# Optimization experiments

Measured on AMD Instinct MI355X. Metric: run time of the kernel, lower is better.

## Reference

```python
import jax, jax.numpy as jnp
import numpy as np

CHUNK_SIZE = 256


def setup_inputs() -> dict:
    key = jax.random.key(0)
    kq, kk, kv = jax.random.split(key, 3)
    b, h, L, d, dv = 2, 16, 4096, 16, 64
    return {
        "q": jax.random.normal(kq, (b, h, L, d), dtype=jnp.float32),
        "k": jax.random.normal(kk, (b, h, L, d), dtype=jnp.float32),
        "v": jax.random.normal(kv, (b, h, L, dv), dtype=jnp.float32),
    }


def reference(q, k, v):
    b, h, L, d = q.shape
    dv = v.shape[-1]
    cs = CHUNK_SIZE
    n = L // cs

    q = q * d ** (-0.5)

    # ---- normalizer z over full sequence ----
    k_cumsum = jnp.cumsum(k, axis=-2)                               # [b,h,L,d]
    kk_cumsum = jnp.cumsum(k[..., :, None] * k[..., None, :], axis=-3)  # [b,h,L,d,d]
    z = (q * k_cumsum).sum(-1)
    z = z + 0.5 * jnp.einsum('bhld,bhle,bhlde->bhl', q, q, kk_cumsum)
    z = z + (jnp.arange(L, dtype=z.dtype) + 1.0)[None, None, :]

    # ---- zeroth-order term ----
    o_const = jnp.cumsum(v, axis=-2)                                # [b,h,L,dv]

    # ---- chunked view ----
    qc = q.reshape(b, h, n, cs, d)
    kc = k.reshape(b, h, n, cs, d)
    vc = v.reshape(b, h, n, cs, dv)

    # intra-chunk quadratic attention: S + 0.5*S^2, causal-masked
    s = jnp.einsum('bhnqd,bhnkd->bhnqk', qc, kc)                    # [b,h,n,cs,cs]
    s = s + 0.5 * s ** 2
    causal_mask = jnp.tril(jnp.ones((cs, cs), dtype=bool))
    s = jnp.where(causal_mask, s, jnp.zeros((), dtype=s.dtype))
    o = jnp.einsum('bhnqk,bhnkf->bhnqf', s, vc)                     # [b,h,n,cs,dv]

    # inter-chunk quadratic state: cumulative K x K x V from previous chunks
    kv_quad = jnp.einsum('bhncd,bhnce,bhncf->bhndef', kc, kc, vc)   # [b,h,n,d,d,dv]
    kv_quad = jnp.cumsum(kv_quad, axis=2)
    kv_quad = jnp.concatenate(
        [jnp.zeros_like(kv_quad[:, :, :1]), kv_quad[:, :, :-1]], axis=2)
    o = o + 0.5 * jnp.einsum('bhndef,bhncd,bhnce->bhncf', kv_quad, qc, qc)

    # inter-chunk linear state: cumulative K x V from previous chunks
    kv_lin = jnp.einsum('bhncd,bhnce->bhnde', kc, vc)               # [b,h,n,d,dv]
    kv_lin = jnp.cumsum(kv_lin, axis=2)
    kv_lin = jnp.concatenate(
        [jnp.zeros_like(kv_lin[:, :, :1]), kv_lin[:, :, :-1]], axis=2)
    o = o + jnp.einsum('bhnde,bhncd->bhnce', kv_lin, qc)

    o = o.reshape(b, h, L, dv) + o_const
    return o / (z[..., None] + 1e-6)
```

## Files before the change

### kernel.cpp

```cpp
#include <hip/hip_runtime.h>
#include <hip/hip_cooperative_groups.h>
#include <cstddef>

#define BH    32
#define LSEQ  4096
#define D     16
#define DV    64
#define CS    256
#define NC    16
#define NF    160
#define NZ    65
#define KSTEPS 5
#define PER   (NZ * NF)

typedef short short8 __attribute__((ext_vector_type(8)));
typedef float f32x4 __attribute__((ext_vector_type(4)));
typedef float f4 __attribute__((ext_vector_type(4)));
typedef unsigned uint4v __attribute__((ext_vector_type(4)));

#define OFF_KBF 0u
#define OFF_VT  (4u*1024u*1024u)
#define OFF_ST  (OFF_VT + (unsigned)(BH*NZ*LSEQ*2))

__device__ __forceinline__ unsigned f2bf(float x) {
  unsigned u = __float_as_uint(x);
  return (u + 0x7FFFu + ((u >> 16) & 1u)) >> 16;
}
__device__ __forceinline__ float bf2f(unsigned short u) {
  return __uint_as_float(((unsigned)u) << 16);
}
__device__ __forceinline__ short8 zero8() {
  short8 z = {0,0,0,0,0,0,0,0};
  return z;
}
__device__ __forceinline__ unsigned cvtpk(float lo, float hi) {
  unsigned r;
  asm("v_cvt_pk_bf16_f32 %0, %1, %2" : "=v"(r) : "v"(lo), "v"(hi));
  return r;
}
__device__ __forceinline__ short8 pk4(unsigned a, unsigned b, unsigned c, unsigned d) {
  uint4v u = {a, b, c, d};
  return __builtin_bit_cast(short8, u);
}

__device__ __forceinline__ unsigned feat_tbl(int f) {
  if (f == 0)  return 16u | (16u << 8);
  if (f <= 16) return (unsigned)(f - 1) | (16u << 8);
  if (f < 137) {
    int p = f - 17, off = 0;
    for (int d = 0; d < 15; ++d) {
      int cnt = 15 - d;
      if (p < off + cnt) return (unsigned)d | ((unsigned)(d + 1 + p - off) << 8);
      off += cnt;
    }
  }
  if (f < 153) {
    int d = f - 137;
    return (unsigned)d | ((unsigned)d << 8) | (1u << 16);
  }
  return 17u | (17u << 8);
}

struct Smem {
  float kxqx[CS][18];
  __align__(16) unsigned short vt[NZ][264];
  union {
    __align__(16) unsigned short stt[NZ][168];
    struct {
      __align__(16) unsigned short ptile[8][640];
      float zline[CS];
    } u;
  } b;
  unsigned tbl[NF];
};

__global__ __launch_bounds__(512, 4) void unified(const float* __restrict__ q,
                                                  const float* __restrict__ k,
                                                  const float* __restrict__ v,
                                                  unsigned* __restrict__ kbf_u32,
                                                  unsigned short* __restrict__ st,
                                                  float* __restrict__ out) {
  __shared__ Smem sm;
  int blk = blockIdx.x, bh = blk >> 4, c = blk & 15;
  int t = threadIdx.x, w = t >> 6, lane = t & 63, quad = lane >> 4, n16 = lane & 15;
  const size_t base = (size_t)bh * LSEQ + (size_t)c * CS;

  {
    const f4* K4 = (const f4*)(k + base * D);
    uint2* kbd2 = (uint2*)(kbf_u32 + base * D / 2);
    for (int idx = t; idx < 1024; idx += 512) {
      f4 kv = K4[idx];
      kbd2[idx] = make_uint2(cvtpk(kv[0], kv[1]), cvtpk(kv[2], kv[3]));
      float* dst = &sm.kxqx[idx >> 2][(idx & 3) * 4];
      *(float2*)dst = make_float2(kv[0], kv[1]);
      *(float2*)(dst + 2) = make_float2(kv[2], kv[3]);
    }
    for (int i = t; i < CS; i += 512)
      *(float2*)&sm.kxqx[i][16] = make_float2(1.f, 0.f);
    const f4* V4 = (const f4*)(v + base * DV);
    for (int idx = t; idx < 2048; idx += 512) {
      int m16 = idx & 15, j0 = (idx >> 4) * 2;
      f4 a  = V4[j0 * 16 + m16];
      f4 bq = V4[j0 * 16 + 16 + m16];
#pragma unroll
      for (int r = 0; r < 4; ++r)
        *(unsigned*)&sm.vt[m16 * 4 + r][j0] = cvtpk(a[r], bq[r]);
    }
    if (t < 128) ((unsigned*)&sm.vt[64][0])[t] = 0x3F803F80u;
    if (t < NF) sm.tbl[t] = feat_tbl(t);
  }
  __syncthreads();

  if (c < 15 && w < 5) {
    unsigned tv0 = sm.tbl[(w * 2 + 0) * 16 + n16];
    unsigned tv1 = sm.tbl[(w * 2 + 1) * 16 + n16];
    int d0 = tv0 & 255, e0 = (tv0 >> 8) & 255;
    int d1 = tv1 & 255, e1 = (tv1 >> 8) & 255;
    f32x4 acc[2][5];
#pragma unroll
    for (int mm = 0; mm < 2; ++mm)
#pragma unroll
      for (int nt = 0; nt < 5; ++nt) acc[mm][nt] = (f32x4){0.f, 0.f, 0.f, 0.f};
    for (int jt = 0; jt < 8; ++jt) {
      float x0[8], x1[8];
#pragma unroll
      for (int i = 0; i < 8; ++i) {
        const float* kr = &sm.kxqx[jt * 32 + quad * 8 + i][0];
        x0[i] = kr[d0] * kr[e0];
        x1[i] = kr[d1] * kr[e1];
      }
      short8 afr0 = pk4(cvtpk(x0[0], x0[1]), cvtpk(x0[2], x0[3]),
                        cvtpk(x0[4], x0[5]), cvtpk(x0[6], x0[7]));
      short8 afr1 = pk4(cvtpk(x1[0], x1[1]), cvtpk(x1[2], x1[3]),
                        cvtpk(x1[4], x1[5]), cvtpk(x1[6], x1[7]));
#pragma unroll
      for (int nt = 0; nt < 5; ++nt) {
        int ncol = nt * 16 + n16;
        short8 b = zero8();
        if (ncol < NZ) b = *(const short8*)(&sm.vt[ncol][jt * 32 + quad * 8]);
        acc[0][nt] = __builtin_amdgcn_mfma_f32_16x16x32_bf16(afr0, b, acc[0][nt], 0, 0, 0);
        acc[1][nt] = __builtin_amdgcn_mfma_f32_16x16x32_bf16(afr1, b, acc[1][nt], 0, 0, 0);
      }
    }
    unsigned short* stc = st + (size_t)(bh * NC + c) * PER;
#pragma unroll
    for (int mm = 0; mm < 2; ++mm) {
      int feat0 = (w * 2 + mm) * 16 + quad * 4;
      float sc[4];
#pragma unroll
      for (int r = 0; r < 4; ++r)
        sc[r] = (feat0 + r >= 137 && feat0 + r < 153) ? 0.5f : 1.0f;
#pragma unroll
      for (int nt = 0; nt < 5; ++nt) {
        int col = nt * 16 + n16;
        if (col < NZ) {
          unsigned lo = cvtpk(acc[mm][nt][0] * sc[0], acc[mm][nt][1] * sc[1]);
          unsigned hi = cvtpk(acc[mm][nt][2] * sc[2], acc[mm][nt][3] * sc[3]);
          *(uint2*)(stc + (size_t)col * NF + feat0) = make_uint2(lo, hi);
        }
      }
    }
  }
  __syncthreads();

  {
    const f4* Q4 = (const f4*)(q + base * D);
    for (int idx = t; idx < 1024; idx += 512) {
      f4 qv = Q4[idx] * 0.25f;
      float* dst = &sm.kxqx[idx >> 2][(idx & 3) * 4];
      *(float2*)dst = make_float2(qv[0], qv[1]);
      *(float2*)(dst + 2) = make_float2(qv[2], qv[3]);
    }
  }

  cooperative_groups::this_grid().sync();

  if (c > 0) {
    const unsigned short* stg = st + (size_t)bh * NC * PER;
    float s0[8], s1[8], s2[8];
#pragma unroll
    for (int e = 0; e < 8; ++e) { s0[e] = 0.f; s1[e] = 0.f; s2[e] = 0.f; }
    const int i0 = t * 8, i1 = i0 + 4096, i2 = i0 + 8192;
    const bool h2 = (i2 < PER);
    for (int cc = 0; cc < c; ++cc) {
      const unsigned short* pcc = stg + (size_t)cc * PER;
      short8 a0 = *(const short8*)(pcc + i0);
      short8 a1 = *(const short8*)(pcc + i1);
      short8 a2 = h2 ? *(const short8*)(pcc + i2) : zero8();
#pragma unroll
      for (int e = 0; e < 8; ++e) {
        s0[e] += bf2f((unsigned short)a0[e]);
        s1[e] += bf2f((unsigned short)a1[e]);
        s2[e] += bf2f((unsigned short)a2[e]);
      }
    }
    {
      int col = i0 / NF, ft = i0 - col * NF;
      *(short8*)(&sm.b.stt[col][ft]) =
          pk4(cvtpk(s0[0], s0[1]), cvtpk(s0[2], s0[3]),
              cvtpk(s0[4], s0[5]), cvtpk(s0[6], s0[7]));
      col = i1 / NF; ft = i1 - col * NF;
      *(short8*)(&sm.b.stt[col][ft]) =
          pk4(cvtpk(s1[0], s1[1]), cvtpk(s1[2], s1[3]),
              cvtpk(s1[4], s1[5]), cvtpk(s1[6], s1[7]));
      if (h2) {
        col = i2 / NF; ft = i2 - col * NF;
        *(short8*)(&sm.b.stt[col][ft]) =
            pk4(cvtpk(s2[0], s2[1]), cvtpk(s2[2], s2[3]),
                cvtpk(s2[4], s2[5]), cvtpk(s2[6], s2[7]));
      }
    }
  }
  __syncthreads();

  f32x4 acc[2][5];
#pragma unroll
  for (int mm = 0; mm < 2; ++mm)
#pragma unroll
    for (int nt = 0; nt < 5; ++nt) acc[mm][nt] = (f32x4){0.f, 0.f, 0.f, 0.f};

  if (c > 0) {
    const float* qrow0 = &sm.kxqx[w * 16 + n16][0];
    const float* qrow1 = &sm.kxqx[(15 - w) * 16 + n16][0];
    for (int ks = 0; ks < KSTEPS; ++ks) {
      unsigned tvv[8];
#pragma unroll
      for (int i = 0; i < 8; ++i) tvv[i] = sm.tbl[ks * 32 + quad * 8 + i];
      float x0[8], x1[8];
#pragma unroll
      for (int i = 0; i < 8; ++i) {
        int d = tvv[i] & 255, e = (tvv[i] >> 8) & 255;
        x0[i] = qrow0[d] * qrow0[e];
        x1[i] = qrow1[d] * qrow1[e];
      }
      short8 afr0 = pk4(cvtpk(x0[0], x0[1]), cvtpk(x0[2], x0[3]),
                        cvtpk(x0[4], x0[5]), cvtpk(x0[6], x0[7]));
      short8 afr1 = pk4(cvtpk(x1[0], x1[1]), cvtpk(x1[2], x1[3]),
                        cvtpk(x1[4], x1[5]), cvtpk(x1[6], x1[7]));
#pragma unroll
      for (int nt = 0; nt < 5; ++nt) {
        int ncol = nt * 16 + n16;
        short8 b = zero8();
        if (ncol < NZ) b = *(const short8*)(&sm.b.stt[ncol][ks * 32 + quad * 8]);
        acc[0][nt] = __builtin_amdgcn_mfma_f32_16x16x32_bf16(afr0, b, acc[0][nt], 0, 0, 0);
        acc[1][nt] = __builtin_amdgcn_mfma_f32_16x16x32_bf16(afr1, b, acc[1][nt], 0, 0, 0);
      }
    }
  }
  __syncthreads();

  const unsigned short* kbc = (const unsigned short*)kbf_u32 + base * D;
  unsigned short* pw = &sm.b.u.ptile[w][0];
  short8 ones;
#pragma unroll
  for (int i = 0; i < 8; ++i) ones[i] = (short)0x3F80;

#pragma unroll
  for (int mm = 0; mm < 2; ++mm) {
    const int s = mm ? (15 - w) : w;
    short8 qf = zero8();
    if (quad < 2) {
      const float2* qr = (const float2*)&sm.kxqx[s * 16 + n16][quad * 8];
      float2 q0 = qr[0], q1 = qr[1], q2 = qr[2], q3 = qr[3];
      qf = pk4(cvtpk(q0.x, q0.y), cvtpk(q1.x, q1.y),
               cvtpk(q2.x, q2.y), cvtpk(q3.x, q3.y));
    }
    const int ntiles = (s >> 1) + 1;
    for (int jt = 0; jt < ntiles; ++jt) {
      short8 kb[2];
#pragma unroll
      for (int ntk = 0; ntk < 2; ++ntk) {
        short8 b = zero8();
        if (quad < 2)
          b = *(const short8*)(kbc + (size_t)(jt * 32 + ntk * 16 + n16) * D + quad * 8);
        kb[ntk] = b;
      }
      f32x4 zf = (f32x4){0.f, 0.f, 0.f, 0.f};
      f32x4 sres[2];
      sres[0] = __builtin_amdgcn_mfma_f32_16x16x32_bf16(qf, kb[0], zf, 0, 0, 0);
      sres[1] = __builtin_amdgcn_mfma_f32_16x16x32_bf16(qf, kb[1], zf, 0, 0, 0);
      const bool last = (jt == ntiles - 1);
#pragma unroll
      for (int ntk = 0; ntk < 2; ++ntk) {
        float ph[4];
#pragma unroll
        for (int r = 0; r < 4; ++r) {
          float sv = sres[ntk][r];
          float phi = fmaf(sv, fmaf(0.5f, sv, 1.0f), 1.0f);
          if (last) {
            int qrow_g = s * 16 + quad * 4 + r;
            int kcol_g = jt * 32 + ntk * 16 + n16;
            if (kcol_g > qrow_g) phi = 0.f;
          }
          ph[r] = phi;
        }
        unsigned u01 = cvtpk(ph[0], ph[1]);
        unsigned u23 = cvtpk(ph[2], ph[3]);
        int rb = (quad * 4) * 40 + ntk * 16 + n16;
        pw[rb      ] = (unsigned short)u01;
        pw[rb +  40] = (unsigned short)(u01 >> 16);
        pw[rb +  80] = (unsigned short)u23;
        pw[rb + 120] = (unsigned short)(u23 >> 16);
      }
      short8 pa = *(const short8*)(pw + n16 * 40 + quad * 8);
#pragma unroll
      for (int nt = 0; nt < 5; ++nt) {
        int ncol = nt * 16 + n16;
        short8 b;
        if (ncol < 64)       b = *(const short8*)(&sm.vt[ncol][jt * 32 + quad * 8]);
        else if (ncol == 64) b = ones;
        else                 b = zero8();
        acc[mm][nt] = __builtin_amdgcn_mfma_f32_16x16x32_bf16(pa, b, acc[mm][nt], 0, 0, 0);
      }
    }
  }

  if (n16 == 0) {
#pragma unroll
    for (int mm = 0; mm < 2; ++mm) {
      int s = mm ? (15 - w) : w;
#pragma unroll
      for (int r = 0; r < 4; ++r)
        sm.b.u.zline[s * 16 + quad * 4 + r] = acc[mm][4][r];
    }
  }
  float* oc = out + base * DV;
#pragma unroll
  for (int mm = 0; mm < 2; ++mm) {
    int s = mm ? (15 - w) : w;
#pragma unroll
    for (int r = 0; r < 4; ++r) {
      int qrow = s * 16 + quad * 4 + r;
      float inv = __builtin_amdgcn_rcpf(sm.b.u.zline[qrow] + 1e-6f);
#pragma unroll
      for (int nt = 0; nt < 4; ++nt)
        oc[(size_t)qrow * DV + nt * 16 + n16] = acc[mm][nt][r] * inv;
    }
  }
}

__global__ __launch_bounds__(320) void pass_a(const float* __restrict__ k,
                                              const float* __restrict__ v,
                                              unsigned* __restrict__ kbf_u32,
                                              unsigned* __restrict__ vt_u32,
                                              unsigned short* __restrict__ st) {
  __shared__ float kx[CS][18];
  __shared__ __align__(16) unsigned short vt_lds[NZ][264];
  __shared__ unsigned tbl[NF];
  int blk = blockIdx.x, bh = blk >> 4, c = blk & 15;
  int t = threadIdx.x, w = t >> 6, lane = t & 63, quad = lane >> 4, n16 = lane & 15;
  {
    const float2* kc2 = (const float2*)(k + ((size_t)bh * LSEQ + c * CS) * D);
    unsigned* kbd = kbf_u32 + ((size_t)bh * LSEQ + c * CS) * D / 2;
    for (int i = t; i < 2048; i += 320) {
      float2 v2 = kc2[i];
      kbd[i] = f2bf(v2.x) | (f2bf(v2.y) << 16);
      int j = i >> 3, dd = (i & 7) * 2;
      kx[j][dd] = v2.x; kx[j][dd + 1] = v2.y;
    }
    for (int i = t; i < CS; i += 320) { kx[i][16] = 1.f; kx[i][17] = 0.f; }
  }
  {
    const float* vb = v + ((size_t)bh * LSEQ + c * CS) * DV;
    for (int i = t; i < CS * DV; i += 320) {
      int j = i >> 6, f = i & 63;
      vt_lds[f][j] = (unsigned short)f2bf(vb[i]);
    }
    for (int i = t; i < CS; i += 320) vt_lds[64][i] = (unsigned short)0x3F80;
  }
  if (t < NF) tbl[t] = feat_tbl(t);
  __syncthreads();
  {
    unsigned* vtg = vt_u32 + (size_t)bh * NZ * (LSEQ / 2) + c * (CS / 2);
    for (int i = t; i < NZ * (CS / 2); i += 320) {
      int f = i >> 7, jp = (i & 127) * 2;
      vtg[(size_t)f * (LSEQ / 2) + (i & 127)] =
          (unsigned)vt_lds[f][jp] | ((unsigned)vt_lds[f][jp + 1] << 16);
    }
  }
  f32x4 acc[2][5];
#pragma unroll
  for (int mm = 0; mm < 2; ++mm)
#pragma unroll
    for (int nt = 0; nt < 5; ++nt) acc[mm][nt] = (f32x4){0.f, 0.f, 0.f, 0.f};
  for (int jt = 0; jt < 8; ++jt) {
    short8 afr[2];
#pragma unroll
    for (int mm = 0; mm < 2; ++mm) {
      int feat = (w * 2 + mm) * 16 + n16;
      unsigned tv = tbl[feat];
      int d = tv & 255, e = (tv >> 8) & 255;
      short8 a;
#pragma unroll
      for (int i = 0; i < 8; ++i) {
        int jj = jt * 32 + quad * 8 + i;
        a[i] = (short)f2bf(kx[jj][d] * kx[jj][e]);
      }
      afr[mm] = a;
    }
#pragma unroll
    for (int nt = 0; nt < 5; ++nt) {
      int ncol = nt * 16 + n16;
      short8 b = zero8();
      if (ncol < NZ) b = *(const short8*)(&vt_lds[ncol][jt * 32 + quad * 8]);
      acc[0][nt] = __builtin_amdgcn_mfma_f32_16x16x32_bf16(afr[0], b, acc[0][nt], 0, 0, 0);
      acc[1][nt] = __builtin_amdgcn_mfma_f32_16x16x32_bf16(afr[1], b, acc[1][nt], 0, 0, 0);
    }
  }
  unsigned short* stc = st + (size_t)(bh * NC + c) * PER;
#pragma unroll
  for (int mm = 0; mm < 2; ++mm)
#pragma unroll
    for (int nt = 0; nt < 5; ++nt) {
      int col = nt * 16 + n16;
      if (col < NZ) {
        unsigned lo = f2bf(acc[mm][nt][0]) | (f2bf(acc[mm][nt][1]) << 16);
        unsigned hi = f2bf(acc[mm][nt][2]) | (f2bf(acc[mm][nt][3]) << 16);
        int feat0 = (w * 2 + mm) * 16 + quad * 4;
        *(uint2*)(stc + (size_t)col * NF + feat0) = make_uint2(lo, hi);
      }
    }
}

__global__ __launch_bounds__(256) void pass_b(unsigned short* __restrict__ st) {
  const int TOT = BH * PER;
  int idx = blockIdx.x * 256 + threadIdx.x;
  if (idx >= TOT) return;
  int bh = idx / PER, r = idx - bh * PER;
  unsigned short* p = st + (size_t)bh * NC * PER + r;
  float run = 0.f;
#pragma unroll
  for (int c = 0; c < NC; ++c) {
    unsigned short uv = p[(size_t)c * PER];
    float val = bf2f(uv);
    p[(size_t)c * PER] = (unsigned short)f2bf(run);
    run += val;
  }
}

__global__ __launch_bounds__(512) void pass_c(const float* __restrict__ q,
                                              const unsigned short* __restrict__ kbf,
                                              const unsigned short* __restrict__ vt,
                                              const unsigned short* __restrict__ st,
                                              float* __restrict__ out) {
  __shared__ float qx[CS][18];
  __shared__ unsigned tbl[NF];
  __shared__ __align__(16) unsigned short ptile[8][32 * 40];
  __shared__ float zline[CS];
  int blk = blockIdx.x, bh = blk >> 4, c = blk & 15;
  const size_t base = (size_t)bh * LSEQ + (size_t)c * CS;
  const float* qc = q + base * D;
  int t = threadIdx.x, w = t >> 6, lane = t & 63, quad = lane >> 4, n16 = lane & 15;
  for (int i = t; i < CS * D; i += 512) {
    int row = i >> 4, dd = i & 15;
    qx[row][dd] = qc[i] * 0.25f;
  }
  for (int i = t; i < CS; i += 512) { qx[i][16] = 1.f; qx[i][17] = 0.f; }
  if (t < NF) tbl[t] = feat_tbl(t);
  __syncthreads();
  f32x4 acc[2][5];
#pragma unroll
  for (int mm = 0; mm < 2; ++mm)
#pragma unroll
    for (int nt = 0; nt < 5; ++nt) acc[mm][nt] = (f32x4){0.f, 0.f, 0.f, 0.f};
  if (c > 0) {
    const unsigned short* stc = st + (size_t)(bh * NC + c) * PER;
    for (int ks = 0; ks < KSTEPS; ++ks) {
      short8 afr[2];
#pragma unroll
      for (int mm = 0; mm < 2; ++mm) {
        const float* qrow = qx[(w * 2 + mm) * 16 + n16];
        short8 a;
#pragma unroll
        for (int i = 0; i < 8; ++i) {
          int f = ks * 32 + quad * 8 + i;
          unsigned tv = tbl[f];
          float val = qrow[tv & 255] * qrow[(tv >> 8) & 255];
          if (tv & 0x10000u) val *= 0.5f;
          a[i] = (short)f2bf(val);
        }
        afr[mm] = a;
      }
#pragma unroll
      for (int nt = 0; nt < 5; ++nt) {
        int ncol = nt * 16 + n16;
        short8 b = zero8();
        if (ncol < NZ) b = *(const short8*)(stc + (size_t)ncol * NF + ks * 32 + quad * 8);
        acc[0][nt] = __builtin_amdgcn_mfma_f32_16x16x32_bf16(afr[0], b, acc[0][nt], 0, 0, 0);
        acc[1][nt] = __builtin_amdgcn_mfma_f32_16x16x32_bf16(afr[1], b, acc[1][nt], 0, 0, 0);
      }
    }
  }
  short8 qfr[2];
#pragma unroll
  for (int mm = 0; mm < 2; ++mm) {
    int m = (w * 2 + mm) * 16 + n16;
    short8 a = zero8();
    if (quad < 2) {
#pragma unroll
      for (int i = 0; i < 8; ++i) a[i] = (short)f2bf(qx[m][quad * 8 + i]);
    }
    qfr[mm] = a;
  }
  const unsigned short* kbc = kbf + base * D;
  const unsigned short* vtb = vt + (size_t)bh * NZ * LSEQ + (size_t)c * CS;
  unsigned short* pw = &ptile[w][0];
  short8 ones;
#pragma unroll
  for (int i = 0; i < 8; ++i) ones[i] = (short)0x3F80;
  for (int jt = 0; jt <= w; ++jt) {
    short8 kb[2];
#pragma unroll
    for (int ntk = 0; ntk < 2; ++ntk) {
      short8 b = zero8();
      if (quad < 2)
        b = *(const short8*)(kbc + (size_t)(jt * 32 + ntk * 16 + n16) * D + quad * 8);
      kb[ntk] = b;
    }
    f32x4 zf = (f32x4){0.f, 0.f, 0.f, 0.f};
    f32x4 s[2][2];
#pragma unroll
    for (int mm = 0; mm < 2; ++mm)
#pragma unroll
      for (int ntk = 0; ntk < 2; ++ntk)
        s[mm][ntk] = __builtin_amdgcn_mfma_f32_16x16x32_bf16(qfr[mm], kb[ntk], zf, 0, 0, 0);
    bool diag = (jt == w);
#pragma unroll
    for (int mm = 0; mm < 2; ++mm)
#pragma unroll
      for (int ntk = 0; ntk < 2; ++ntk)
#pragma unroll
        for (int r = 0; r < 4; ++r) {
          float sv = s[mm][ntk][r];
          float phi = fmaf(0.5f * sv, sv, sv) + 1.0f;
          if (diag) {
            int qrow = mm * 16 + quad * 4 + r;
            int kcol = ntk * 16 + n16;
            if (kcol > qrow) phi = 0.f;
          }
          pw[(mm * 16 + quad * 4 + r) * 40 + ntk * 16 + n16] = (unsigned short)f2bf(phi);
        }
    short8 pa[2];
#pragma unroll
    for (int mm = 0; mm < 2; ++mm)
      pa[mm] = *(const short8*)(pw + (mm * 16 + n16) * 40 + quad * 8);
#pragma unroll
    for (int nt = 0; nt < 5; ++nt) {
      int ncol = nt * 16 + n16;
      short8 b;
      if (ncol < 64)       b = *(const short8*)(vtb + (size_t)ncol * LSEQ + jt * 32 + quad * 8);
      else if (ncol == 64) b = ones;
      else                 b = zero8();
      acc[0][nt] = __builtin_amdgcn_mfma_f32_16x16x32_bf16(pa[0], b, acc[0][nt], 0, 0, 0);
      acc[1][nt] = __builtin_amdgcn_mfma_f32_16x16x32_bf16(pa[1], b, acc[1][nt], 0, 0, 0);
    }
  }
  if (n16 == 0) {
#pragma unroll
    for (int mm = 0; mm < 2; ++mm)
#pragma unroll
      for (int r = 0; r < 4; ++r)
        zline[(w * 2 + mm) * 16 + quad * 4 + r] = acc[mm][4][r];
  }
  float* oc = out + base * DV;
#pragma unroll
  for (int mm = 0; mm < 2; ++mm)
#pragma unroll
    for (int r = 0; r < 4; ++r) {
      int qrow = (w * 2 + mm) * 16 + quad * 4 + r;
      float inv = 1.0f / (zline[qrow] + 1e-6f);
#pragma unroll
      for (int nt = 0; nt < 4; ++nt)
        oc[(size_t)qrow * DV + nt * 16 + n16] = acc[mm][nt][r] * inv;
    }
}

extern "C" void kernel_launch(void* const* d_in, const int* in_sizes, int n_in,
                              void* d_out, int out_size, void* d_ws, size_t ws_size,
                              hipStream_t stream) {
  (void)in_sizes; (void)n_in; (void)out_size; (void)ws_size;
  const float* q = (const float*)d_in[0];
  const float* k = (const float*)d_in[1];
  const float* v = (const float*)d_in[2];
  float* out = (float*)d_out;
  char* wsb = (char*)d_ws;
  unsigned*       kbf32 = (unsigned*)(wsb + OFF_KBF);
  unsigned short* kbf   = (unsigned short*)(wsb + OFF_KBF);
  unsigned*       vt32  = (unsigned*)(wsb + OFF_VT);
  unsigned short* vtp   = (unsigned short*)(wsb + OFF_VT);
  unsigned short* stp   = (unsigned short*)(wsb + OFF_ST);

  int nb = 0;
  hipError_t oe = hipOccupancyMaxActiveBlocksPerMultiprocessor(
      &nb, reinterpret_cast<const void*>(unified), 512, 0);
  if (oe == hipSuccess && nb >= 2) {
    void* args[] = {(void*)&q, (void*)&k, (void*)&v,
                    (void*)&kbf32, (void*)&stp, (void*)&out};
    hipLaunchCooperativeKernel(reinterpret_cast<const void*>(unified),
                               dim3(BH * NC), dim3(512), args, 0, stream);
  } else {
    pass_a<<<BH * NC, 320, 0, stream>>>(k, v, kbf32, vt32, stp);
    pass_b<<<1300, 256, 0, stream>>>(stp);
    pass_c<<<BH * NC, 512, 0, stream>>>(q, kbf, vtp, stp, out);
  }
}
```

Before: 135.2 us.

## Move intra-chunk attention before grid sync and rebalance state work across waves

The intra-chunk causal attention now runs before the cooperative grid barrier, computed from K held in LDS instead of a bf16 K copy in global memory, so the global K write is dropped. Q fragments are loaded straight from global into registers at kernel start. Chunk-state feature tiles are spread over all 8 waves (waves 0-1 take two tiles), and query-row slices are reassigned so causal work is balanced per wave. The prefix-sum loop over earlier chunk states is software-pipelined with one-ahead loads. The accumulators now stay live across the grid sync, which raises register pressure.

```diff
diff --git a/kernel.cpp b/kernel.cpp
--- a/kernel.cpp
+++ b/kernel.cpp
@@ -84,13 +84,28 @@
   int blk = blockIdx.x, bh = blk >> 4, c = blk & 15;
   int t = threadIdx.x, w = t >> 6, lane = t & 63, quad = lane >> 4, n16 = lane & 15;
   const size_t base = (size_t)bh * LSEQ + (size_t)c * CS;
+  (void)kbf_u32;
+
+  const int s0 = (w < 2) ? 2 * w : (w + 2);
+  const int s1 = (w < 2) ? 2 * w + 1 : (17 - w);
+
+  short8 qf[2] = {zero8(), zero8()};
+  if (quad < 2) {
+#pragma unroll
+    for (int mm = 0; mm < 2; ++mm) {
+      int s = mm ? s1 : s0;
+      const f4* qp = (const f4*)(q + (base + (size_t)(s * 16 + n16)) * D + quad * 8);
+      f4 qa = qp[0] * 0.25f;
+      f4 qb = qp[1] * 0.25f;
+      qf[mm] = pk4(cvtpk(qa[0], qa[1]), cvtpk(qa[2], qa[3]),
+                   cvtpk(qb[0], qb[1]), cvtpk(qb[2], qb[3]));
+    }
+  }
 
   {
     const f4* K4 = (const f4*)(k + base * D);
-    uint2* kbd2 = (uint2*)(kbf_u32 + base * D / 2);
     for (int idx = t; idx < 1024; idx += 512) {
       f4 kv = K4[idx];
-      kbd2[idx] = make_uint2(cvtpk(kv[0], kv[1]), cvtpk(kv[2], kv[3]));
       float* dst = &sm.kxqx[idx >> 2][(idx & 3) * 4];
       *(float2*)dst = make_float2(kv[0], kv[1]);
       *(float2*)(dst + 2) = make_float2(kv[2], kv[3]);
@@ -111,41 +126,34 @@
   }
   __syncthreads();
 
-  if (c < 15 && w < 5) {
-    unsigned tv0 = sm.tbl[(w * 2 + 0) * 16 + n16];
-    unsigned tv1 = sm.tbl[(w * 2 + 1) * 16 + n16];
-    int d0 = tv0 & 255, e0 = (tv0 >> 8) & 255;
-    int d1 = tv1 & 255, e1 = (tv1 >> 8) & 255;
-    f32x4 acc[2][5];
-#pragma unroll
-    for (int mm = 0; mm < 2; ++mm)
-#pragma unroll
-      for (int nt = 0; nt < 5; ++nt) acc[mm][nt] = (f32x4){0.f, 0.f, 0.f, 0.f};
-    for (int jt = 0; jt < 8; ++jt) {
-      float x0[8], x1[8];
-#pragma unroll
-      for (int i = 0; i < 8; ++i) {
-        const float* kr = &sm.kxqx[jt * 32 + quad * 8 + i][0];
-        x0[i] = kr[d0] * kr[e0];
-        x1[i] = kr[d1] * kr[e1];
-      }
-      short8 afr0 = pk4(cvtpk(x0[0], x0[1]), cvtpk(x0[2], x0[3]),
-                        cvtpk(x0[4], x0[5]), cvtpk(x0[6], x0[7]));
-      short8 afr1 = pk4(cvtpk(x1[0], x1[1]), cvtpk(x1[2], x1[3]),
-                        cvtpk(x1[4], x1[5]), cvtpk(x1[6], x1[7]));
-#pragma unroll
-      for (int nt = 0; nt < 5; ++nt) {
-        int ncol = nt * 16 + n16;
-        short8 b = zero8();
-        if (ncol < NZ) b = *(const short8*)(&sm.vt[ncol][jt * 32 + quad * 8]);
-        acc[0][nt] = __builtin_amdgcn_mfma_f32_16x16x32_bf16(afr0, b, acc[0][nt], 0, 0, 0);
-        acc[1][nt] = __builtin_amdgcn_mfma_f32_16x16x32_bf16(afr1, b, acc[1][nt], 0, 0, 0);
-      }
-    }
+  if (c < 15) {
+    const int ntt = (w < 2) ? 2 : 1;
     unsigned short* stc = st + (size_t)(bh * NC + c) * PER;
-#pragma unroll
-    for (int mm = 0; mm < 2; ++mm) {
-      int feat0 = (w * 2 + mm) * 16 + quad * 4;
+    for (int tt = 0; tt < ntt; ++tt) {
+      const int T = tt ? (w + 8) : w;
+      unsigned tv = sm.tbl[T * 16 + n16];
+      int d0 = tv & 255, e0 = (tv >> 8) & 255;
+      f32x4 acc5[5];
+#pragma unroll
+      for (int nt = 0; nt < 5; ++nt) acc5[nt] = (f32x4){0.f, 0.f, 0.f, 0.f};
+      for (int jt = 0; jt < 8; ++jt) {
+        float x[8];
+#pragma unroll
+        for (int i = 0; i < 8; ++i) {
+          const float* kr = &sm.kxqx[jt * 32 + quad * 8 + i][0];
+          x[i] = kr[d0] * kr[e0];
+        }
+        short8 afr = pk4(cvtpk(x[0], x[1]), cvtpk(x[2], x[3]),
+                         cvtpk(x[4], x[5]), cvtpk(x[6], x[7]));
+#pragma unroll
+        for (int nt = 0; nt < 5; ++nt) {
+          int ncol = nt * 16 + n16;
+          short8 b = zero8();
+          if (ncol < NZ) b = *(const short8*)(&sm.vt[ncol][jt * 32 + quad * 8]);
+          acc5[nt] = __builtin_amdgcn_mfma_f32_16x16x32_bf16(afr, b, acc5[nt], 0, 0, 0);
+        }
+      }
+      const int feat0 = T * 16 + quad * 4;
       float sc[4];
 #pragma unroll
       for (int r = 0; r < 4; ++r)
@@ -154,9 +162,80 @@
       for (int nt = 0; nt < 5; ++nt) {
         int col = nt * 16 + n16;
         if (col < NZ) {
-          unsigned lo = cvtpk(acc[mm][nt][0] * sc[0], acc[mm][nt][1] * sc[1]);
-          unsigned hi = cvtpk(acc[mm][nt][2] * sc[2], acc[mm][nt][3] * sc[3]);
+          unsigned lo = cvtpk(acc5[nt][0] * sc[0], acc5[nt][1] * sc[1]);
+          unsigned hi = cvtpk(acc5[nt][2] * sc[2], acc5[nt][3] * sc[3]);
           *(uint2*)(stc + (size_t)col * NF + feat0) = make_uint2(lo, hi);
+        }
+      }
+    }
+  }
+
+  f32x4 accC[2][5];
+#pragma unroll
+  for (int mm = 0; mm < 2; ++mm)
+#pragma unroll
+    for (int nt = 0; nt < 5; ++nt) accC[mm][nt] = (f32x4){0.f, 0.f, 0.f, 0.f};
+
+  {
+    unsigned short* pw = &sm.b.u.ptile[w][0];
+    short8 ones;
+#pragma unroll
+    for (int i = 0; i < 8; ++i) ones[i] = (short)0x3F80;
+
+#pragma unroll
+    for (int mm = 0; mm < 2; ++mm) {
+      const int s = mm ? s1 : s0;
+      const int ntiles = (s >> 1) + 1;
+      for (int jt = 0; jt < ntiles; ++jt) {
+        short8 kb[2];
+#pragma unroll
+        for (int ntk = 0; ntk < 2; ++ntk) {
+          short8 b = zero8();
+          if (quad < 2) {
+            const float2* kr =
+                (const float2*)&sm.kxqx[jt * 32 + ntk * 16 + n16][quad * 8];
+            float2 k0 = kr[0], k1 = kr[1], k2 = kr[2], k3 = kr[3];
+            b = pk4(cvtpk(k0.x, k0.y), cvtpk(k1.x, k1.y),
+                    cvtpk(k2.x, k2.y), cvtpk(k3.x, k3.y));
+          }
+          kb[ntk] = b;
+        }
+        f32x4 zf = (f32x4){0.f, 0.f, 0.f, 0.f};
+        f32x4 sres[2];
+        sres[0] = __builtin_amdgcn_mfma_f32_16x16x32_bf16(qf[mm], kb[0], zf, 0, 0, 0);
+        sres[1] = __builtin_amdgcn_mfma_f32_16x16x32_bf16(qf[mm], kb[1], zf, 0, 0, 0);
+        const bool last = (jt == ntiles - 1);
+#pragma unroll
+        for (int ntk = 0; ntk < 2; ++ntk) {
+          float ph[4];
+#pragma unroll
+          for (int r = 0; r < 4; ++r) {
+            float sv = sres[ntk][r];
+            float phi = fmaf(sv, fmaf(0.5f, sv, 1.0f), 1.0f);
+            if (last) {
+              int qrow_g = s * 16 + quad * 4 + r;
+              int kcol_g = jt * 32 + ntk * 16 + n16;
+              if (kcol_g > qrow_g) phi = 0.f;
+            }
+            ph[r] = phi;
+          }
+          unsigned u01 = cvtpk(ph[0], ph[1]);
+          unsigned u23 = cvtpk(ph[2], ph[3]);
+          int rb = (quad * 4) * 40 + ntk * 16 + n16;
+          pw[rb      ] = (unsigned short)u01;
+          pw[rb +  40] = (unsigned short)(u01 >> 16);
+          pw[rb +  80] = (unsigned short)u23;
+          pw[rb + 120] = (unsigned short)(u23 >> 16);
+        }
+        short8 pa = *(const short8*)(pw + n16 * 40 + quad * 8);
+#pragma unroll
+        for (int nt = 0; nt < 5; ++nt) {
+          int ncol = nt * 16 + n16;
+          short8 b;
+          if (ncol < 64)       b = *(const short8*)(&sm.vt[ncol][jt * 32 + quad * 8]);
+          else if (ncol == 64) b = ones;
+          else                 b = zero8();
+          accC[mm][nt] = __builtin_amdgcn_mfma_f32_16x16x32_bf16(pa, b, accC[mm][nt], 0, 0, 0);
         }
       }
     }
@@ -177,51 +256,55 @@
 
   if (c > 0) {
     const unsigned short* stg = st + (size_t)bh * NC * PER;
-    float s0[8], s1[8], s2[8];
-#pragma unroll
-    for (int e = 0; e < 8; ++e) { s0[e] = 0.f; s1[e] = 0.f; s2[e] = 0.f; }
+    float sa0[8], sa1[8], sa2[8];
+#pragma unroll
+    for (int e = 0; e < 8; ++e) { sa0[e] = 0.f; sa1[e] = 0.f; sa2[e] = 0.f; }
     const int i0 = t * 8, i1 = i0 + 4096, i2 = i0 + 8192;
     const bool h2 = (i2 < PER);
-    for (int cc = 0; cc < c; ++cc) {
-      const unsigned short* pcc = stg + (size_t)cc * PER;
-      short8 a0 = *(const short8*)(pcc + i0);
-      short8 a1 = *(const short8*)(pcc + i1);
-      short8 a2 = h2 ? *(const short8*)(pcc + i2) : zero8();
+    short8 a0 = *(const short8*)(stg + i0);
+    short8 a1 = *(const short8*)(stg + i1);
+    short8 a2 = h2 ? *(const short8*)(stg + i2) : zero8();
+    for (int cc = 1; cc < c; ++cc) {
+      const unsigned short* pn = stg + (size_t)cc * PER;
+      short8 b0 = *(const short8*)(pn + i0);
+      short8 b1 = *(const short8*)(pn + i1);
+      short8 b2 = h2 ? *(const short8*)(pn + i2) : zero8();
 #pragma unroll
       for (int e = 0; e < 8; ++e) {
-        s0[e] += bf2f((unsigned short)a0[e]);
-        s1[e] += bf2f((unsigned short)a1[e]);
-        s2[e] += bf2f((unsigned short)a2[e]);
-      }
+        sa0[e] += bf2f((unsigned short)a0[e]);
+        sa1[e] += bf2f((unsigned short)a1[e]);
+        sa2[e] += bf2f((unsigned short)a2[e]);
+      }
+      a0 = b0; a1 = b1; a2 = b2;
+    }
+#pragma unroll
+    for (int e = 0; e < 8; ++e) {
+      sa0[e] += bf2f((unsigned short)a0[e]);
+      sa1[e] += bf2f((unsigned short)a1[e]);
+      sa2[e] += bf2f((unsigned short)a2[e]);
     }
     {
       int col = i0 / NF, ft = i0 - col * NF;
       *(short8*)(&sm.b.stt[col][ft]) =
-          pk4(cvtpk(s0[0], s0[1]), cvtpk(s0[2], s0[3]),
-              cvtpk(s0[4], s0[5]), cvtpk(s0[6], s0[7]));
+          pk4(cvtpk(sa0[0], sa0[1]), cvtpk(sa0[2], sa0[3]),
+              cvtpk(sa0[4], sa0[5]), cvtpk(sa0[6], sa0[7]));
       col = i1 / NF; ft = i1 - col * NF;
       *(short8*)(&sm.b.stt[col][ft]) =
-          pk4(cvtpk(s1[0], s1[1]), cvtpk(s1[2], s1[3]),
-              cvtpk(s1[4], s1[5]), cvtpk(s1[6], s1[7]));
+          pk4(cvtpk(sa1[0], sa1[1]), cvtpk(sa1[2], sa1[3]),
+              cvtpk(sa1[4], sa1[5]), cvtpk(sa1[6], sa1[7]));
       if (h2) {
         col = i2 / NF; ft = i2 - col * NF;
         *(short8*)(&sm.b.stt[col][ft]) =
-            pk4(cvtpk(s2[0], s2[1]), cvtpk(s2[2], s2[3]),
-                cvtpk(s2[4], s2[5]), cvtpk(s2[6], s2[7]));
+            pk4(cvtpk(sa2[0], sa2[1]), cvtpk(sa2[2], sa2[3]),
+                cvtpk(sa2[4], sa2[5]), cvtpk(sa2[6], sa2[7]));
       }
     }
   }
   __syncthreads();
 
-  f32x4 acc[2][5];
-#pragma unroll
-  for (int mm = 0; mm < 2; ++mm)
-#pragma unroll
-    for (int nt = 0; nt < 5; ++nt) acc[mm][nt] = (f32x4){0.f, 0.f, 0.f, 0.f};
-
   if (c > 0) {
-    const float* qrow0 = &sm.kxqx[w * 16 + n16][0];
-    const float* qrow1 = &sm.kxqx[(15 - w) * 16 + n16][0];
+    const float* qrow0 = &sm.kxqx[s0 * 16 + n16][0];
+    const float* qrow1 = &sm.kxqx[s1 * 16 + n16][0];
     for (int ks = 0; ks < KSTEPS; ++ks) {
       unsigned tvv[8];
 #pragma unroll
@@ -242,99 +325,33 @@
         int ncol = nt * 16 + n16;
         short8 b = zero8();
         if (ncol < NZ) b = *(const short8*)(&sm.b.stt[ncol][ks * 32 + quad * 8]);
-        acc[0][nt] = __builtin_amdgcn_mfma_f32_16x16x32_bf16(afr0, b, acc[0][nt], 0, 0, 0);
-        acc[1][nt] = __builtin_amdgcn_mfma_f32_16x16x32_bf16(afr1, b, acc[1][nt], 0, 0, 0);
+        accC[0][nt] = __builtin_amdgcn_mfma_f32_16x16x32_bf16(afr0, b, accC[0][nt], 0, 0, 0);
+        accC[1][nt] = __builtin_amdgcn_mfma_f32_16x16x32_bf16(afr1, b, accC[1][nt], 0, 0, 0);
       }
     }
   }
   __syncthreads();
 
-  const unsigned short* kbc = (const unsigned short*)kbf_u32 + base * D;
-  unsigned short* pw = &sm.b.u.ptile[w][0];
-  short8 ones;
-#pragma unroll
-  for (int i = 0; i < 8; ++i) ones[i] = (short)0x3F80;
-
+  if (n16 == 0) {
+#pragma unroll
+    for (int mm = 0; mm < 2; ++mm) {
+      int s = mm ? s1 : s0;
+#pragma unroll
+      for (int r = 0; r < 4; ++r)
+        sm.b.u.zline[s * 16 + quad * 4 + r] = accC[mm][4][r];
+    }
+  }
+  float* oc = out + base * DV;
 #pragma unroll
   for (int mm = 0; mm < 2; ++mm) {
-    const int s = mm ? (15 - w) : w;
-    short8 qf = zero8();
-    if (quad < 2) {
-      const float2* qr = (const float2*)&sm.kxqx[s * 16 + n16][quad * 8];
-      float2 q0 = qr[0], q1 = qr[1], q2 = qr[2], q3 = qr[3];
-      qf = pk4(cvtpk(q0.x, q0.y), cvtpk(q1.x, q1.y),
-               cvtpk(q2.x, q2.y), cvtpk(q3.x, q3.y));
-    }
-    const int ntiles = (s >> 1) + 1;
-    for (int jt = 0; jt < ntiles; ++jt) {
-      short8 kb[2];
-#pragma unroll
-      for (int ntk = 0; ntk < 2; ++ntk) {
-        short8 b = zero8();
-        if (quad < 2)
-          b = *(const short8*)(kbc + (size_t)(jt * 32 + ntk * 16 + n16) * D + quad * 8);
-        kb[ntk] = b;
-      }
-      f32x4 zf = (f32x4){0.f, 0.f, 0.f, 0.f};
-      f32x4 sres[2];
-      sres[0] = __builtin_amdgcn_mfma_f32_16x16x32_bf16(qf, kb[0], zf, 0, 0, 0);
-      sres[1] = __builtin_amdgcn_mfma_f32_16x16x32_bf16(qf, kb[1], zf, 0, 0, 0);
-      const bool last = (jt == ntiles - 1);
-#pragma unroll
-      for (int ntk = 0; ntk < 2; ++ntk) {
-        float ph[4];
-#pragma unroll
-        for (int r = 0; r < 4; ++r) {
-          float sv = sres[ntk][r];
-          float phi = fmaf(sv, fmaf(0.5f, sv, 1.0f), 1.0f);
-          if (last) {
-            int qrow_g = s * 16 + quad * 4 + r;
-            int kcol_g = jt * 32 + ntk * 16 + n16;
-            if (kcol_g > qrow_g) phi = 0.f;
-          }
-          ph[r] = phi;
-        }
-        unsigned u01 = cvtpk(ph[0], ph[1]);
-        unsigned u23 = cvtpk(ph[2], ph[3]);
-        int rb = (quad * 4) * 40 + ntk * 16 + n16;
-        pw[rb      ] = (unsigned short)u01;
-        pw[rb +  40] = (unsigned short)(u01 >> 16);
-        pw[rb +  80] = (unsigned short)u23;
-        pw[rb + 120] = (unsigned short)(u23 >> 16);
-      }
-      short8 pa = *(const short8*)(pw + n16 * 40 + quad * 8);
-#pragma unroll
-      for (int nt = 0; nt < 5; ++nt) {
-        int ncol = nt * 16 + n16;
-        short8 b;
-        if (ncol < 64)       b = *(const short8*)(&sm.vt[ncol][jt * 32 + quad * 8]);
-        else if (ncol == 64) b = ones;
-        else                 b = zero8();
-        acc[mm][nt] = __builtin_amdgcn_mfma_f32_16x16x32_bf16(pa, b, acc[mm][nt], 0, 0, 0);
-      }
-    }
-  }
-
-  if (n16 == 0) {
-#pragma unroll
-    for (int mm = 0; mm < 2; ++mm) {
-      int s = mm ? (15 - w) : w;
-#pragma unroll
-      for (int r = 0; r < 4; ++r)
-        sm.b.u.zline[s * 16 + quad * 4 + r] = acc[mm][4][r];
-    }
-  }
-  float* oc = out + base * DV;
-#pragma unroll
-  for (int mm = 0; mm < 2; ++mm) {
-    int s = mm ? (15 - w) : w;
+    int s = mm ? s1 : s0;
 #pragma unroll
     for (int r = 0; r < 4; ++r) {
       int qrow = s * 16 + quad * 4 + r;
       float inv = __builtin_amdgcn_rcpf(sm.b.u.zline[qrow] + 1e-6f);
 #pragma unroll
       for (int nt = 0; nt < 4; ++nt)
-        oc[(size_t)qrow * DV + nt * 16 + n16] = acc[mm][nt][r] * inv;
+        oc[(size_t)qrow * DV + nt * 16 + n16] = accC[mm][nt][r] * inv;
     }
   }
 }
```

Measured after the change: 134.2 us. Within noise of the previous version (-0.7%).
